# Optimization experiments

Measured on AMD Instinct MI355X. Metric: run time of the kernel, lower is better.

## Reference

```python
import math
import jax, jax.numpy as jnp
import numpy as np

S = 32.0
M1 = 1.0
M2 = 0.5
M3 = 0.0
MM = M2 * math.sin(math.pi - M2)
NUM_CLASSES = 100000
FEATURES = 512
BATCH = 512


def setup_inputs() -> dict:
    key = jax.random.key(0)
    k1, k2, k3 = jax.random.split(key, 3)
    inputs = jax.random.normal(k1, (BATCH, FEATURES), dtype=jnp.float32)
    labels = jax.random.randint(k2, (BATCH,), 0, NUM_CLASSES, dtype=jnp.int64)
    # xavier_uniform on [num_classes, features]
    limit = math.sqrt(6.0 / (NUM_CLASSES + FEATURES))
    weight = jax.random.uniform(k3, (NUM_CLASSES, FEATURES), minval=-limit, maxval=limit, dtype=jnp.float32)
    return {"inputs": inputs, "labels": labels, "weight": weight}


def reference(inputs, labels, weight):
    # L2 normalize (torch F.normalize uses eps=1e-12 clamp on norm)
    inp_n = inputs / jnp.maximum(jnp.linalg.norm(inputs, axis=1, keepdims=True), 1e-12)
    w_n = weight / jnp.maximum(jnp.linalg.norm(weight, axis=1, keepdims=True), 1e-12)
    cos_in = jnp.clip(inp_n @ w_n.T, -1.0 + 1e-6, 1.0 - 1e-6)  # [N, C]
    theta_in = jnp.arccos(cos_in)
    one_hot = jax.nn.one_hot(labels, NUM_CLASSES, dtype=cos_in.dtype)
    theta_out = theta_in + (theta_in * (M1 - 1.0) + M2) * one_hot
    cos_out = jnp.where(
        theta_out < math.pi,
        jnp.cos(theta_out) - M3 * one_hot,
        cos_in - MM * one_hot - M3 * one_hot,
    )
    outs = S * cos_out  # [N, C]
    # mean cross-entropy
    logp = jax.nn.log_softmax(outs, axis=1)
    n = jnp.arange(BATCH)
    loss = -jnp.mean(logp[n, labels])
    target_cos_in = cos_in[n, labels][:, None]
    target_theta_in = theta_in[n, labels][:, None]
    target_cos_out = cos_out[n, labels][:, None]
    return loss, outs, target_cos_in, target_theta_in, target_cos_out
```

## Files before the change

### kernel.cpp

```cpp
#include <hip/hip_runtime.h>
#include <stdint.h>

#define BATCH 512
#define FEAT 512
#define NCLS 100000
#define BM 128
#define BN 128
#define BK 64
#define NBLK_N 782
#define NBLK (NBLK_N * 4)
#define NCHUNK (NBLK_N * 2)
#define SCALE_S 32.0f
#define MARGIN 0.5f
#define MM_CONST 0.23971276930210156f
#define PI_F 3.14159265358979f

typedef unsigned int u32;
typedef unsigned short u16;
typedef __bf16 bf16x8 __attribute__((ext_vector_type(8)));
typedef float f32x4 __attribute__((ext_vector_type(4)));

__device__ __forceinline__ u16 f2bf(float f) {
  u32 u = __float_as_uint(f);
  u += 0x7fffu + ((u >> 16) & 1u);
  return (u16)(u >> 16);
}

__device__ __forceinline__ void async_copy16(const void* g, void* l) {
  __builtin_amdgcn_global_load_lds((const __attribute__((address_space(1))) u32*)g,
                                   (__attribute__((address_space(3))) u32*)l,
                                   16, 0, 0);
}

__device__ __forceinline__ float block_reduce_sum(float v, float* sbuf) {
  for (int off = 1; off < 64; off <<= 1) v += __shfl_xor(v, off, 64);
  int wid = threadIdx.x >> 6, lane = threadIdx.x & 63;
  __syncthreads();
  if (lane == 0) sbuf[wid] = v;
  __syncthreads();
  return sbuf[0] + sbuf[1] + sbuf[2] + sbuf[3];
}

__global__ __launch_bounds__(256) void norm_all_kernel(const float* __restrict__ inputs,
                                                       const float* __restrict__ weight,
                                                       u16* __restrict__ dstA,
                                                       u16* __restrict__ dstB,
                                                       float* __restrict__ out0) {
  if (blockIdx.x == 0 && threadIdx.x == 0) out0[0] = 0.0f;
  const int lane = threadIdx.x & 63;
  const int gw = (blockIdx.x * 256 + threadIdx.x) >> 6;
  const int nw = gridDim.x * 4;
  for (int row = gw; row < BATCH + NCLS; row += nw) {
    const float* src;
    u16* dst;
    if (row < BATCH) {
      src = inputs + (size_t)row * FEAT;
      dst = dstA + (size_t)row * FEAT;
    } else {
      src = weight + (size_t)(row - BATCH) * FEAT;
      dst = dstB + (size_t)(row - BATCH) * FEAT;
    }
    const float4* p4 = (const float4*)src;
    float4 a = p4[lane];
    float4 b = p4[lane + 64];
    float ss = a.x * a.x + a.y * a.y + a.z * a.z + a.w * a.w +
               b.x * b.x + b.y * b.y + b.z * b.z + b.w * b.w;
#pragma unroll
    for (int off = 1; off < 64; off <<= 1) ss += __shfl_xor(ss, off, 64);
    float inv = 1.0f / fmaxf(sqrtf(ss), 1e-12f);
    ushort4 oa, ob;
    oa.x = f2bf(a.x * inv); oa.y = f2bf(a.y * inv);
    oa.z = f2bf(a.z * inv); oa.w = f2bf(a.w * inv);
    ob.x = f2bf(b.x * inv); ob.y = f2bf(b.y * inv);
    ob.z = f2bf(b.z * inv); ob.w = f2bf(b.w * inv);
    ((ushort4*)dst)[lane] = oa;
    ((ushort4*)dst)[lane + 64] = ob;
  }
}

__global__ __launch_bounds__(256, 3) void gemm_kernel(const u16* __restrict__ A,
                                                      const u16* __restrict__ B,
                                                      const int* __restrict__ labels,
                                                      float* __restrict__ outs,
                                                      float* __restrict__ partials) {
  __shared__ __align__(16) u16 sB0[BN * BK];
  __shared__ __align__(16) u16 sB1[BN * BK];
  __shared__ int sLab[BM];

  const int tid = threadIdx.x;
  const int lane = tid & 63;
  const int wid = tid >> 6;
  const int waveM = wid >> 1, waveN = wid & 1;
  const int orig = blockIdx.x;
  const int L = (orig & 7) * (NBLK / 8) + (orig >> 3);
  const int bm = L & 3, bn = L >> 2;
  const int quad = lane >> 4, l15 = lane & 15;

  if (tid < BM) sLab[tid] = labels[bm * BM + tid];

  const u16* gB[4];
#pragma unroll
  for (int rd = 0; rd < 4; ++rd) {
    int idx = rd * 256 + tid;
    int r = idx >> 3;
    int cb = (idx & 7) ^ (r & 7);
    int brow = bn * BN + r;
    if (brow >= NCLS) brow = NCLS - 1;
    gB[rd] = B + (size_t)brow * FEAT + cb * 8;
  }
  const u16* gA = A + (size_t)(bm * BM + waveM * 64 + l15) * FEAT;

  f32x4 acc[4][4] = {};

#define STAGE_B(SBUF, KT)                                         \
  do {                                                            \
    _Pragma("unroll") for (int rd = 0; rd < 4; ++rd)              \
        async_copy16(gB[rd] + (KT)*BK, &(SBUF)[(rd * 256 + tid) * 8]); \
  } while (0)

#define K_STEP(SBUF_CUR, SBUF_NXT, KT, LAST)                                     \
  do {                                                                           \
    bf16x8 aF[4][2];                                                             \
    _Pragma("unroll") for (int mi = 0; mi < 4; ++mi)                             \
        _Pragma("unroll") for (int ks = 0; ks < 2; ++ks)                         \
            aF[mi][ks] = *(const bf16x8*)(gA + (size_t)mi * 16 * FEAT +          \
                                          (KT)*BK + (ks * 4 + quad) * 8);        \
    __builtin_amdgcn_sched_barrier(0);      \
    if (!(LAST)) {                                                               \
      STAGE_B(SBUF_NXT, (KT) + 1);                                              \
           \
      asm volatile("s_waitcnt vmcnt(12)" ::: "memory");                          \
    } else {                                                                     \
      asm volatile("s_waitcnt vmcnt(8)" ::: "memory");            \
    }                                                                            \
    asm volatile("s_barrier" ::: "memory");      \
    _Pragma("unroll") for (int ks = 0; ks < 2; ++ks) {                           \
      int j0 = ks * 4 + quad;                                                    \
      bf16x8 bF[4];                                                              \
      _Pragma("unroll") for (int ni = 0; ni < 4; ++ni) {                         \
        int r = waveN * 64 + ni * 16 + l15;                                      \
        bF[ni] = *(const bf16x8*)&(SBUF_CUR)[(r * 8 + (j0 ^ (r & 7))) * 8];     \
      }                                                                          \
      _Pragma("unroll") for (int mi = 0; mi < 4; ++mi)                           \
          _Pragma("unroll") for (int ni = 0; ni < 4; ++ni)                       \
              acc[mi][ni] = __builtin_amdgcn_mfma_f32_16x16x32_bf16(             \
                  aF[mi][ks], bF[ni], acc[mi][ni], 0, 0, 0);                     \
    }                                                                            \
    asm volatile("s_barrier" ::: "memory");   \
  } while (0)

  STAGE_B(sB0, 0);
  __syncthreads();

  K_STEP(sB0, sB1, 0, false);
  K_STEP(sB1, sB0, 1, false);
  K_STEP(sB0, sB1, 2, false);
  K_STEP(sB1, sB0, 3, false);
  K_STEP(sB0, sB1, 4, false);
  K_STEP(sB1, sB0, 5, false);
  K_STEP(sB0, sB1, 6, false);
  K_STEP(sB1, sB0, 7, true);

#undef K_STEP
#undef STAGE_B

#pragma unroll
  for (int mi = 0; mi < 4; ++mi) {
#pragma unroll
    for (int reg = 0; reg < 4; ++reg) {
      int rloc = waveM * 64 + mi * 16 + quad * 4 + reg;
      int rg = bm * BM + rloc;
      int lab = sLab[rloc];
      float vals[4];
      float rmax = -1e30f;
#pragma unroll
      for (int ni = 0; ni < 4; ++ni) {
        int cg = bn * BN + waveN * 64 + ni * 16 + l15;
        float v = acc[mi][ni][reg];
        v = fminf(fmaxf(v, -1.0f + 1e-6f), 1.0f - 1e-6f);
        if (cg == lab) {
          float th = acosf(v) + MARGIN;
          v = (th < PI_F) ? cosf(th) : (v - MM_CONST);
        }
        v *= SCALE_S;
        if (cg < NCLS)
          outs[(size_t)rg * NCLS + cg] = v;
        else
          v = -1e30f;
        vals[ni] = v;
        rmax = fmaxf(rmax, v);
      }
#pragma unroll
      for (int off = 1; off < 16; off <<= 1) rmax = fmaxf(rmax, __shfl_xor(rmax, off, 64));
      float rsum = 0.f;
#pragma unroll
      for (int ni = 0; ni < 4; ++ni) rsum += __expf(vals[ni] - rmax);
#pragma unroll
      for (int off = 1; off < 16; off <<= 1) rsum += __shfl_xor(rsum, off, 64);
      if (l15 == 0) {
        float* p = partials + ((size_t)rg * NCHUNK + (bn * 2 + waveN)) * 2;
        p[0] = rmax;
        p[1] = rsum;
      }
    }
  }
}

__global__ __launch_bounds__(256) void combine_kernel(const float* __restrict__ partials,
                                                      const float* __restrict__ outs,
                                                      const int* __restrict__ labels,
                                                      const float* __restrict__ inputs,
                                                      const float* __restrict__ weight,
                                                      float* __restrict__ out0,
                                                      float* __restrict__ tdst) {
  __shared__ float sbuf[4];
  __shared__ float smx[4], slx[4];
  int r = blockIdx.x, tid = threadIdx.x;
  int lab = labels[r];

  const float2* px = (const float2*)(inputs + (size_t)r * FEAT);
  const float2* pw = (const float2*)(weight + (size_t)lab * FEAT);
  float2 x = px[tid], w = pw[tid];
  float dot = block_reduce_sum(x.x * w.x + x.y * w.y, sbuf);
  float sx = block_reduce_sum(x.x * x.x + x.y * x.y, sbuf);
  float sw = block_reduce_sum(w.x * w.x + w.y * w.y, sbuf);

  const float* p = partials + (size_t)r * NCHUNK * 2;
  float m = -1e30f, l = 0.f;
  for (int i = tid; i < NCHUNK; i += 256) {
    float mi = p[2 * i], li = p[2 * i + 1];
    if (mi > m) { l = l * __expf(m - mi) + li; m = mi; }
    else l += li * __expf(mi - m);
  }
  for (int off = 1; off < 64; off <<= 1) {
    float mo = __shfl_xor(m, off, 64);
    float lo = __shfl_xor(l, off, 64);
    if (mo > m) { l = l * __expf(m - mo) + lo; m = mo; }
    else l += lo * __expf(mo - m);
  }
  int wv = tid >> 6, lane = tid & 63;
  if (lane == 0) { smx[wv] = m; slx[wv] = l; }
  __syncthreads();
  if (tid == 0) {
    for (int wq = 1; wq < 4; ++wq) {
      float mo = smx[wq], lo = slx[wq];
      if (mo > m) { l = l * __expf(m - mo) + lo; m = mo; }
      else l += lo * __expf(mo - m);
    }
    float lse = m + logf(l);
    float tgt = outs[(size_t)r * NCLS + lab];
    atomicAdd(out0, (lse - tgt) * (1.0f / BATCH));

    float inv = 1.0f / (fmaxf(sqrtf(sx), 1e-12f) * fmaxf(sqrtf(sw), 1e-12f));
    float ci = fminf(fmaxf(dot * inv, -1.0f + 1e-6f), 1.0f - 1e-6f);
    float th = acosf(ci);
    float t2 = th + MARGIN;
    float co = (t2 < PI_F) ? cosf(t2) : (ci - MM_CONST);
    tdst[r] = ci;
    tdst[BATCH + r] = th;
    tdst[2 * BATCH + r] = co;
  }
}

extern "C" void kernel_launch(void* const* d_in, const int* in_sizes, int n_in,
                              void* d_out, int out_size, void* d_ws, size_t ws_size,
                              hipStream_t stream) {
  const float* inputs = (const float*)d_in[0];
  const int* labels = (const int*)d_in[1];
  const float* weight = (const float*)d_in[2];
  float* out = (float*)d_out;
  float* outs = out + 1;
  float* tdst = out + 1 + (size_t)BATCH * NCLS;

  char* ws = (char*)d_ws;
  u16* wsA = (u16*)ws;
  u16* wsB = (u16*)(ws + 524288);
  float* partials = (float*)(ws + 524288 + 102400000);

  norm_all_kernel<<<2048, 256, 0, stream>>>(inputs, weight, wsA, wsB, out);
  gemm_kernel<<<NBLK, 256, 0, stream>>>(wsA, wsB, labels, outs, partials);
  combine_kernel<<<BATCH, 256, 0, stream>>>(partials, outs, labels, inputs, weight, out, tdst);
}
```

Before: 507.3 us.

## Triple-buffer B tiles with register double-buffered A and fixed-max softmax

Moves the GEMM main loop from a two-stage to a three-stage LDS ring for B, and double-buffers the A fragments in registers so that loads for the next two k-steps overlap the current MFMAs. The epilogue drops the per-chunk running max because logits are bounded by S: it sums exp(v - S) directly, writes a single partial per chunk, and streams the logits out with nontemporal stores. The combine kernel becomes a plain sum plus a log. The extra buffer raises LDS use per block, which may lower occupancy below the launch-bounds target of 3.

Result: slower. 563.4 us (+11.1%).

```diff
diff --git a/kernel.cpp b/kernel.cpp
--- a/kernel.cpp
+++ b/kernel.cpp
@@ -85,6 +85,7 @@
                                                       float* __restrict__ partials) {
   __shared__ __align__(16) u16 sB0[BN * BK];
   __shared__ __align__(16) u16 sB1[BN * BK];
+  __shared__ __align__(16) u16 sB2[BN * BK];
   __shared__ int sLab[BM];
 
   const int tid = threadIdx.x;
@@ -111,58 +112,80 @@
   const u16* gA = A + (size_t)(bm * BM + waveM * 64 + l15) * FEAT;
 
   f32x4 acc[4][4] = {};
-
-#define STAGE_B(SBUF, KT)                                         \
-  do {                                                            \
-    _Pragma("unroll") for (int rd = 0; rd < 4; ++rd)              \
-        async_copy16(gB[rd] + (KT)*BK, &(SBUF)[(rd * 256 + tid) * 8]); \
+  bf16x8 a0[4][2], a1[4][2];
+
+#define STAGE_B(SBUF, KT)                                                   \
+  do {                                                                      \
+    _Pragma("unroll") for (int rd = 0; rd < 4; ++rd)                        \
+        async_copy16(gB[rd] + (KT)*BK, &(SBUF)[(rd * 256 + tid) * 8]);      \
   } while (0)
 
-#define K_STEP(SBUF_CUR, SBUF_NXT, KT, LAST)                                     \
-  do {                                                                           \
-    bf16x8 aF[4][2];                                                             \
-    _Pragma("unroll") for (int mi = 0; mi < 4; ++mi)                             \
-        _Pragma("unroll") for (int ks = 0; ks < 2; ++ks)                         \
-            aF[mi][ks] = *(const bf16x8*)(gA + (size_t)mi * 16 * FEAT +          \
-                                          (KT)*BK + (ks * 4 + quad) * 8);        \
-    __builtin_amdgcn_sched_barrier(0);      \
-    if (!(LAST)) {                                                               \
-      STAGE_B(SBUF_NXT, (KT) + 1);                                              \
-           \
-      asm volatile("s_waitcnt vmcnt(12)" ::: "memory");                          \
-    } else {                                                                     \
-      asm volatile("s_waitcnt vmcnt(8)" ::: "memory");            \
-    }                                                                            \
-    asm volatile("s_barrier" ::: "memory");      \
-    _Pragma("unroll") for (int ks = 0; ks < 2; ++ks) {                           \
-      int j0 = ks * 4 + quad;                                                    \
-      bf16x8 bF[4];                                                              \
-      _Pragma("unroll") for (int ni = 0; ni < 4; ++ni) {                         \
-        int r = waveN * 64 + ni * 16 + l15;                                      \
-        bF[ni] = *(const bf16x8*)&(SBUF_CUR)[(r * 8 + (j0 ^ (r & 7))) * 8];     \
-      }                                                                          \
-      _Pragma("unroll") for (int mi = 0; mi < 4; ++mi)                           \
-          _Pragma("unroll") for (int ni = 0; ni < 4; ++ni)                       \
-              acc[mi][ni] = __builtin_amdgcn_mfma_f32_16x16x32_bf16(             \
-                  aF[mi][ks], bF[ni], acc[mi][ni], 0, 0, 0);                     \
-    }                                                                            \
-    asm volatile("s_barrier" ::: "memory");   \
+#define LOAD_A(AREG, KT)                                                    \
+  do {                                                                      \
+    _Pragma("unroll") for (int mi = 0; mi < 4; ++mi)                        \
+        _Pragma("unroll") for (int ks = 0; ks < 2; ++ks)                    \
+            AREG[mi][ks] = *(const bf16x8*)(gA + (size_t)mi * 16 * FEAT +   \
+                                            (KT)*BK + (ks * 4 + quad) * 8); \
   } while (0)
 
+#define COMPUTE(SBUF, AREG)                                                 \
+  do {                                                                      \
+    _Pragma("unroll") for (int ks = 0; ks < 2; ++ks) {                      \
+      int j0 = ks * 4 + quad;                                               \
+      bf16x8 bF[4];                                                         \
+      _Pragma("unroll") for (int ni = 0; ni < 4; ++ni) {                    \
+        int r = waveN * 64 + ni * 16 + l15;                                 \
+        bF[ni] = *(const bf16x8*)&(SBUF)[(r * 8 + (j0 ^ (r & 7))) * 8];     \
+      }                                                                     \
+      _Pragma("unroll") for (int mi = 0; mi < 4; ++mi)                      \
+          _Pragma("unroll") for (int ni = 0; ni < 4; ++ni)                  \
+              acc[mi][ni] = __builtin_amdgcn_mfma_f32_16x16x32_bf16(        \
+                  AREG[mi][ks], bF[ni], acc[mi][ni], 0, 0, 0);              \
+    }                                                                       \
+  } while (0)
+
+#define SCHED0 __builtin_amdgcn_sched_barrier(0)
+#define VMCNT(N) asm volatile("s_waitcnt vmcnt(" #N ")" ::: "memory")
+#define BAR asm volatile("s_barrier" ::: "memory")
+
   STAGE_B(sB0, 0);
+  STAGE_B(sB1, 1);
+  LOAD_A(a0, 0);
   __syncthreads();
 
-  K_STEP(sB0, sB1, 0, false);
-  K_STEP(sB1, sB0, 1, false);
-  K_STEP(sB0, sB1, 2, false);
-  K_STEP(sB1, sB0, 3, false);
-  K_STEP(sB0, sB1, 4, false);
-  K_STEP(sB1, sB0, 5, false);
-  K_STEP(sB0, sB1, 6, false);
-  K_STEP(sB1, sB0, 7, true);
-
-#undef K_STEP
+  LOAD_A(a1, 1); SCHED0; STAGE_B(sB2, 2); SCHED0;
+  COMPUTE(sB0, a0);
+  BAR;
+  LOAD_A(a0, 2); SCHED0; STAGE_B(sB0, 3); SCHED0;
+  VMCNT(16);
+  COMPUTE(sB1, a1);
+  BAR;
+  LOAD_A(a1, 3); SCHED0; STAGE_B(sB1, 4); SCHED0;
+  VMCNT(16); BAR;
+  COMPUTE(sB2, a0);
+  BAR;
+  LOAD_A(a0, 4); SCHED0; STAGE_B(sB2, 5); SCHED0;
+  VMCNT(16); BAR;
+  COMPUTE(sB0, a1);
+  BAR;
+  LOAD_A(a1, 5); SCHED0; STAGE_B(sB0, 6); SCHED0;
+  VMCNT(16); BAR;
+  COMPUTE(sB1, a0);
+  BAR;
+  LOAD_A(a0, 6); SCHED0; STAGE_B(sB1, 7); SCHED0;
+  VMCNT(16); BAR;
+  COMPUTE(sB2, a1);
+  BAR;
+  LOAD_A(a1, 7); SCHED0;
+  VMCNT(12); BAR;
+  COMPUTE(sB0, a0);
+  BAR;
+  VMCNT(0); BAR;
+  COMPUTE(sB1, a1);
+
 #undef STAGE_B
+#undef LOAD_A
+#undef COMPUTE
 
 #pragma unroll
   for (int mi = 0; mi < 4; ++mi) {
@@ -171,8 +194,7 @@
       int rloc = waveM * 64 + mi * 16 + quad * 4 + reg;
       int rg = bm * BM + rloc;
       int lab = sLab[rloc];
-      float vals[4];
-      float rmax = -1e30f;
+      float rsum = 0.f;
 #pragma unroll
       for (int ni = 0; ni < 4; ++ni) {
         int cg = bn * BN + waveN * 64 + ni * 16 + l15;
@@ -183,25 +205,14 @@
           v = (th < PI_F) ? cosf(th) : (v - MM_CONST);
         }
         v *= SCALE_S;
-        if (cg < NCLS)
-          outs[(size_t)rg * NCLS + cg] = v;
-        else
-          v = -1e30f;
-        vals[ni] = v;
-        rmax = fmaxf(rmax, v);
+        if (cg < NCLS) {
+          __builtin_nontemporal_store(v, &outs[(size_t)rg * NCLS + cg]);
+          rsum += __expf(v - SCALE_S);
+        }
       }
 #pragma unroll
-      for (int off = 1; off < 16; off <<= 1) rmax = fmaxf(rmax, __shfl_xor(rmax, off, 64));
-      float rsum = 0.f;
-#pragma unroll
-      for (int ni = 0; ni < 4; ++ni) rsum += __expf(vals[ni] - rmax);
-#pragma unroll
       for (int off = 1; off < 16; off <<= 1) rsum += __shfl_xor(rsum, off, 64);
-      if (l15 == 0) {
-        float* p = partials + ((size_t)rg * NCHUNK + (bn * 2 + waveN)) * 2;
-        p[0] = rmax;
-        p[1] = rsum;
-      }
+      if (l15 == 0) partials[(size_t)rg * NCHUNK + (bn * 2 + waveN)] = rsum;
     }
   }
 }
@@ -214,7 +225,6 @@
                                                       float* __restrict__ out0,
                                                       float* __restrict__ tdst) {
   __shared__ float sbuf[4];
-  __shared__ float smx[4], slx[4];
   int r = blockIdx.x, tid = threadIdx.x;
   int lab = labels[r];
 
@@ -225,29 +235,13 @@
   float sx = block_reduce_sum(x.x * x.x + x.y * x.y, sbuf);
   float sw = block_reduce_sum(w.x * w.x + w.y * w.y, sbuf);
 
-  const float* p = partials + (size_t)r * NCHUNK * 2;
-  float m = -1e30f, l = 0.f;
-  for (int i = tid; i < NCHUNK; i += 256) {
-    float mi = p[2 * i], li = p[2 * i + 1];
-    if (mi > m) { l = l * __expf(m - mi) + li; m = mi; }
-    else l += li * __expf(mi - m);
-  }
-  for (int off = 1; off < 64; off <<= 1) {
-    float mo = __shfl_xor(m, off, 64);
-    float lo = __shfl_xor(l, off, 64);
-    if (mo > m) { l = l * __expf(m - mo) + lo; m = mo; }
-    else l += lo * __expf(mo - m);
-  }
-  int wv = tid >> 6, lane = tid & 63;
-  if (lane == 0) { smx[wv] = m; slx[wv] = l; }
-  __syncthreads();
+  const float* p = partials + (size_t)r * NCHUNK;
+  float l = 0.f;
+  for (int i = tid; i < NCHUNK; i += 256) l += p[i];
+  float lt = block_reduce_sum(l, sbuf);
+
   if (tid == 0) {
-    for (int wq = 1; wq < 4; ++wq) {
-      float mo = smx[wq], lo = slx[wq];
-      if (mo > m) { l = l * __expf(m - mo) + lo; m = mo; }
-      else l += lo * __expf(mo - m);
-    }
-    float lse = m + logf(l);
+    float lse = SCALE_S + logf(lt);
     float tgt = outs[(size_t)r * NCLS + lab];
     atomicAdd(out0, (lse - tgt) * (1.0f / BATCH));
 
```
